# Kernel tuning notes

Hardware: AMD Instinct MI355X
Metric: run time of the kernel (lower is better)

The kernel has to match this reference:

```python
import jax, jax.numpy as jnp
import numpy as np

B, L = 1, 2048
D_MODEL, D_STATE, D_CONV, EXPAND = 512, 16, 4, 2
D_INNER = D_MODEL * EXPAND
EPS = 1e-10  # clamp used by the torch reference


def setup_inputs() -> dict:
    key = jax.random.key(0)
    ks = jax.random.split(key, 8)
    s = lambda fan: 1.0 / np.sqrt(fan)
    x = jax.random.normal(ks[0], (B, L, D_MODEL), jnp.float32)
    # Weights stored in (in, out) layout: y = x @ W  (equivalent to torch Linear with W.T)
    W_in = jax.random.normal(ks[1], (D_MODEL, 2 * D_INNER), jnp.float32) * s(D_MODEL)
    conv_w = jax.random.normal(ks[2], (D_INNER, 1, D_CONV), jnp.float32) * s(D_CONV)  # depthwise (O, I/groups, K)
    conv_b = jax.random.normal(ks[3], (D_INNER,), jnp.float32) * 0.01
    W_xproj = jax.random.normal(ks[4], (D_INNER, 2 * D_STATE + 1), jnp.float32) * s(D_INNER)
    dt_w = jax.random.normal(ks[5], (D_INNER,), jnp.float32) * 0.1  # Linear(1, d_inner) weight, squeezed
    dt_b = jax.random.normal(ks[6], (D_INNER,), jnp.float32) * 0.1 - 2.0  # keep delta smallish
    A_log = jnp.log(jnp.arange(1, D_STATE + 1, dtype=jnp.float32))
    D = jnp.ones((D_INNER,), jnp.float32)
    W_out = jax.random.normal(ks[7], (D_INNER, D_MODEL), jnp.float32) * s(D_INNER)
    return {"x": x, "W_in": W_in, "conv_w": conv_w, "conv_b": conv_b,
            "W_xproj": W_xproj, "dt_w": dt_w, "dt_b": dt_b,
            "A_log": A_log, "D": D, "W_out": W_out}


def reference(x, W_in, conv_w, conv_b, W_xproj, dt_w, dt_b, A_log, D, W_out):
    d_inner, _, d_conv = conv_w.shape
    d_state = A_log.shape[0]

    xz = x @ W_in                                    # (B, L, 2*d_inner)
    xs, z = jnp.split(xz, 2, axis=-1)

    # Depthwise causal conv1d: left-pad d_conv-1 == torch pad-both + truncate to L
    xc = jnp.transpose(xs, (0, 2, 1))                # (B, d_inner, L)
    xc = jax.lax.conv_general_dilated(
        xc, conv_w, window_strides=(1,), padding=[(d_conv - 1, 0)],
        feature_group_count=d_inner,
        dimension_numbers=("NCH", "OIH", "NCH")) + conv_b[None, :, None]
    xs = jax.nn.silu(jnp.transpose(xc, (0, 2, 1)))   # (B, L, d_inner)

    xp = xs @ W_xproj                                # (B, L, 2*d_state+1)
    delta = jax.nn.softplus(xp[..., 0:1] * dt_w + dt_b)  # (B, L, d_inner)
    Bp = xp[..., 1:1 + d_state]                      # (B, L, d_state)
    Cp = xp[..., 1 + d_state:]                       # (B, L, d_state)
    A = -jnp.exp(A_log)                              # (d_state,)

    # --- parallel selective scan via cumulative log-sum (faithful to source) ---
    A_bar = jnp.exp(delta[..., None] * A)                            # (B,L,Di,S)
    BX = delta[..., None] * Bp[:, :, None, :] * xs[..., None]        # (B,L,Di,S)
    log_A_bar = jnp.log(jnp.maximum(A_bar, EPS))
    A_cumsum = jnp.exp(jnp.cumsum(log_A_bar, axis=1))
    A_shift = jnp.concatenate([jnp.ones_like(A_cumsum[:, :1]), A_cumsum[:, :-1]], axis=1)
    weighted_BX = BX / jnp.maximum(A_shift, EPS)
    h = A_cumsum * jnp.cumsum(weighted_BX, axis=1) / jnp.maximum(A_bar, EPS)
    y = jnp.einsum("bls,blds->bld", Cp, h) + D * xs                  # (B,L,Di)

    y = y * jax.nn.silu(z)
    return y @ W_out                                                  # (B,L,D)
```

## Files before the change

kernel.cpp:

```cpp
#include <hip/hip_runtime.h>
#include <hip/hip_bf16.h>


#define L_SEQ 2048
#define DM 512
#define DI 1024
#define DS 16
#define NXP 33
#define EPS 1e-10f
#define RCPEPS 1e10f
#define LOG2E 1.44269504088896340736f
#define LN2 0.69314718055994530942f
#define LOG2EPS -33.219280948873623478f

typedef __hip_bfloat16 bf16;
typedef __attribute__((ext_vector_type(8))) short bf16x8v;
typedef __attribute__((ext_vector_type(4))) float f32x4v;
typedef __attribute__((ext_vector_type(4))) unsigned int u32x4v;

__device__ __forceinline__ void st1(float* p, float v) { *p = v; }
__device__ __forceinline__ void st1(bf16* p, float v) { *p = __float2bfloat16(v); }

__device__ __forceinline__ float fexp2(float x) { return __builtin_amdgcn_exp2f(x); }
__device__ __forceinline__ float frcp(float x) { return __builtin_amdgcn_rcpf(x); }

__device__ __forceinline__ void load8(const float* p, float* v) {
  float4 a = *(const float4*)p;
  float4 b = *(const float4*)(p + 4);
  v[0] = a.x; v[1] = a.y; v[2] = a.z; v[3] = a.w;
  v[4] = b.x; v[5] = b.y; v[6] = b.z; v[7] = b.w;
}

__global__ __launch_bounds__(256)
void prep_kernel(const float* __restrict__ W_in, bf16* __restrict__ WinT,
                 const float* __restrict__ x, bf16* __restrict__ xbf) {
  __shared__ float tile[32][33];
  int b = blockIdx.x;
  if (b < 1024) {
    int c0 = (b & 63) * 32, r0 = (b >> 6) * 32;
    int tx = threadIdx.x & 31, ty = threadIdx.x >> 5;
#pragma unroll
    for (int i = 0; i < 4; ++i) {
      int rr = ty + i * 8;
      tile[rr][tx] = W_in[(size_t)(r0 + rr) * (2 * DI) + c0 + tx];
    }
    __syncthreads();
#pragma unroll
    for (int i = 0; i < 4; ++i) {
      int cc = ty + i * 8;
      WinT[(size_t)(c0 + cc) * DM + r0 + tx] = __float2bfloat16(tile[tx][cc]);
    }
  } else {
    int i = (b - 1024) * 256 + threadIdx.x;
    float v[8];
    load8(x + (size_t)i * 8, v);
    bf16 o[8];
#pragma unroll
    for (int j = 0; j < 8; ++j) o[j] = __float2bfloat16(v[j]);
    *(uint4*)(xbf + (size_t)i * 8) = *(uint4*)o;
  }
}

template <int WM, int WN, typename TC>
__global__ __launch_bounds__(256)
void gemm_gl(const bf16* __restrict__ A, const bf16* __restrict__ BT,
             TC* __restrict__ C, int K, int lda, int ldc) {
  constexpr int BM = 2 * WM * 16, BN = 2 * WN * 16;
  __shared__ __align__(16) bf16 As[2][BM * 32];
  __shared__ __align__(16) bf16 Bs[2][BN * 32];
  const int tid = threadIdx.x;
  const int wave = tid >> 6, lane = tid & 63;
  const int q = lane >> 4, r = lane & 15;
  const int wr = wave >> 1, wc = wave & 1;
  const int row0 = blockIdx.y * BM, col0 = blockIdx.x * BN;
  f32x4v acc[WM][WN] = {};
  const int nt = K / 32;

  auto stage = [&](int buf, int t) {
    int k0 = t * 32;
#pragma unroll
    for (int i = 0; i < BM / 64; ++i) {
      int slot = tid + i * 256;
      int row = slot >> 2, seg = slot & 3;
      __builtin_amdgcn_global_load_lds(
          (const __attribute__((address_space(1))) void*)(
              A + (size_t)(row0 + row) * lda + k0 + seg * 8),
          (__attribute__((address_space(3))) void*)&As[buf][row * 32 + seg * 8],
          16, 0, 0);
    }
#pragma unroll
    for (int i = 0; i < BN / 64; ++i) {
      int slot = tid + i * 256;
      int row = slot >> 2, seg = slot & 3;
      __builtin_amdgcn_global_load_lds(
          (const __attribute__((address_space(1))) void*)(
              BT + (size_t)(col0 + row) * K + k0 + seg * 8),
          (__attribute__((address_space(3))) void*)&Bs[buf][row * 32 + seg * 8],
          16, 0, 0);
    }
  };

  stage(0, 0);
  __syncthreads();
  int cur = 0;
  for (int t = 0; t < nt; ++t) {
    if (t + 1 < nt) stage(cur ^ 1, t + 1);
    bf16x8v a[WM], b[WN];
#pragma unroll
    for (int m = 0; m < WM; ++m)
      a[m] = *(const bf16x8v*)&As[cur][(wr * WM * 16 + m * 16 + r) * 32 + q * 8];
#pragma unroll
    for (int n = 0; n < WN; ++n)
      b[n] = *(const bf16x8v*)&Bs[cur][(wc * WN * 16 + n * 16 + r) * 32 + q * 8];
#pragma unroll
    for (int m = 0; m < WM; ++m)
#pragma unroll
      for (int n = 0; n < WN; ++n)
        acc[m][n] = __builtin_amdgcn_mfma_f32_16x16x32_bf16(a[m], b[n],
                                                            acc[m][n], 0, 0, 0);
    __syncthreads();
    cur ^= 1;
  }
#pragma unroll
  for (int m = 0; m < WM; ++m)
#pragma unroll
    for (int n = 0; n < WN; ++n)
#pragma unroll
      for (int reg = 0; reg < 4; ++reg) {
        int mm = row0 + wr * WM * 16 + m * 16 + q * 4 + reg;
        int nn = col0 + wc * WN * 16 + n * 16 + r;
        st1(C + (size_t)mm * ldc + nn, acc[m][n][reg]);
      }
}

__global__ __launch_bounds__(256)
void gemm_xproj_sk(const bf16* __restrict__ A, const float* __restrict__ Wx,
                   float* __restrict__ xpcT) {
  __shared__ __align__(16) bf16 As[64 * 40];
  __shared__ __align__(16) bf16 Bs[64 * 40];
  const int tid = threadIdx.x;
  const int wave = tid >> 6, lane = tid & 63;
  const int q = lane >> 4, r = lane & 15;
  const int row0 = blockIdx.y * 64;
  const int kb = blockIdx.x * 128;
  const int srow = tid >> 2, sseg = tid & 3;
  f32x4v acc[4] = {};
  for (int k0 = kb; k0 < kb + 128; k0 += 32) {
    *(uint4*)&As[srow * 40 + sseg * 8] =
        *(const uint4*)(A + (size_t)(row0 + srow) * DI + k0 + sseg * 8);
    int k = tid >> 3, n0 = (tid & 7) * 8;
#pragma unroll
    for (int j = 0; j < 8; ++j) {
      int n = n0 + j;
      float v = (n < NXP) ? Wx[(size_t)(k0 + k) * NXP + n] : 0.f;
      Bs[n * 40 + k] = __float2bfloat16(v);
    }
    __syncthreads();
    bf16x8v a = *(const bf16x8v*)&As[(wave * 16 + r) * 40 + q * 8];
#pragma unroll
    for (int j = 0; j < 4; ++j) {
      bf16x8v b = *(const bf16x8v*)&Bs[(j * 16 + r) * 40 + q * 8];
      acc[j] = __builtin_amdgcn_mfma_f32_16x16x32_bf16(a, b, acc[j], 0, 0, 0);
    }
    __syncthreads();
  }
#pragma unroll
  for (int j = 0; j < 4; ++j)
#pragma unroll
    for (int reg = 0; reg < 4; ++reg) {
      int m = row0 + wave * 16 + q * 4 + reg;
      int n = j * 16 + r;
      if (n < NXP) atomicAdd(&xpcT[(size_t)n * L_SEQ + m], acc[j][reg]);
    }
}

__global__ __launch_bounds__(256)
void conv_silu_dual(const bf16* __restrict__ xz, const float* __restrict__ conv_w,
                    const float* __restrict__ conv_b, bf16* __restrict__ xs,
                    bf16* __restrict__ xsT, float* __restrict__ xpcT) {
  __shared__ bf16 tile[67][72];
  __shared__ bf16 sout[64][72];
  const int tid = threadIdx.x;
  const int d0 = blockIdx.x * 64, l0 = blockIdx.y * 64;
  {
    int zb = blockIdx.y * gridDim.x + blockIdx.x;
    if (tid < 132) xpcT[(size_t)zb * 132 + tid] = 0.f;
  }
  for (int slot = tid; slot < 67 * 8; slot += 256) {
    int rr = slot >> 3, seg = slot & 7;
    int l = l0 - 3 + rr;
    uint4 v = {0, 0, 0, 0};
    if (l >= 0) v = *(const uint4*)(xz + (size_t)l * (2 * DI) + d0 + seg * 8);
    *(uint4*)&tile[rr][seg * 8] = v;
  }
  __syncthreads();
  {
    int lr = tid >> 3, c0t = (tid & 7) * 8;
#pragma unroll
    for (int half = 0; half < 2; ++half) {
      int lrow = lr + half * 32;
      bf16 o[8];
#pragma unroll
      for (int j = 0; j < 8; ++j) {
        int c = c0t + j;
        float acc = conv_b[d0 + c];
#pragma unroll
        for (int k = 0; k < 4; ++k)
          acc = fmaf(__bfloat162float(tile[lrow + k][c]), conv_w[(d0 + c) * 4 + k], acc);
        float v = acc / (1.f + __expf(-acc));
        o[j] = __float2bfloat16(v);
        sout[c][lrow] = o[j];
      }
      *(uint4*)(xs + (size_t)(l0 + lrow) * DI + d0 + c0t) = *(uint4*)o;
    }
  }
  __syncthreads();
  for (int slot = tid; slot < 64 * 8; slot += 256) {
    int dd = slot >> 3, seg = slot & 7;
    *(uint4*)(xsT + (size_t)(d0 + dd) * L_SEQ + l0 + seg * 8) =
        *(uint4*)&sout[dd][seg * 8];
  }
}

__global__ __launch_bounds__(256)
void gate_wt_kernel(const bf16* __restrict__ yT, const bf16* __restrict__ zbuf,
                    int ldz, bf16* __restrict__ ys,
                    const float* __restrict__ W_out, bf16* __restrict__ WoutT) {
  __shared__ bf16 tile[64][72];
  __shared__ float ttile[32][33];
  if (blockIdx.y >= 16) {
    int tb = (blockIdx.y - 16) * 32 + blockIdx.x;
    int c0 = (tb & 15) * 32, r0 = (tb >> 4) * 32;
    int tx = threadIdx.x & 31, ty = threadIdx.x >> 5;
#pragma unroll
    for (int i = 0; i < 4; ++i) {
      int rr = ty + i * 8;
      ttile[rr][tx] = W_out[(size_t)(r0 + rr) * DM + c0 + tx];
    }
    __syncthreads();
#pragma unroll
    for (int i = 0; i < 4; ++i) {
      int cc = ty + i * 8;
      WoutT[(size_t)(c0 + cc) * DI + r0 + tx] = __float2bfloat16(ttile[tx][cc]);
    }
    return;
  }
  int d0 = blockIdx.y * 64, l0 = blockIdx.x * 64;
#pragma unroll
  for (int it = 0; it < 2; ++it) {
    int slot = threadIdx.x + it * 256;
    int dd = slot >> 3, seg = slot & 7;
    *(uint4*)&tile[dd][seg * 8] = *(const uint4*)(yT + (size_t)(d0 + dd) * L_SEQ + l0 + seg * 8);
  }
  __syncthreads();
#pragma unroll
  for (int it = 0; it < 2; ++it) {
    int slot = threadIdx.x + it * 256;
    int ll = slot >> 3, seg = slot & 7;
    bf16 zt[8];
    *(uint4*)zt = *(const uint4*)(zbuf + (size_t)(l0 + ll) * ldz + d0 + seg * 8);
    bf16 o[8];
#pragma unroll
    for (int j = 0; j < 8; ++j) {
      float yv = __bfloat162float(tile[seg * 8 + j][ll]);
      float zv = __bfloat162float(zt[j]);
      o[j] = __float2bfloat16(yv * zv * frcp(1.f + fexp2(-zv * LOG2E)));
    }
    *(uint4*)(ys + (size_t)(l0 + ll) * DI + d0 + seg * 8) = *(uint4*)o;
  }
}

#define LC 512
#define NW 16
#define SPW 32
#define PSX 513
#define LCP 516

__global__ __launch_bounds__(1024)
void scan_kernel(bf16* __restrict__ xsT, const float* __restrict__ xpcT,
                 const float* __restrict__ dt_w, const float* __restrict__ dt_b,
                 const float* __restrict__ A_log, const float* __restrict__ Dvec) {
  __shared__ float sxpT[NXP * PSX];
  __shared__ float sdt[4 * LCP], sg[4 * LCP], sxs[4 * LCP];
  __shared__ float sys[4 * LCP];
  __shared__ float Wtot[NW][64], Vtot[NW][64];
  const int tid = threadIdx.x;
  const int wave = tid >> 6, lane = tid & 63;
  const int s = lane & 15, dl = lane >> 4;
  const int d0 = blockIdx.x * 4;
  const int base = wave * SPW;
  const float As2 = -expf(A_log[s]) * LOG2E;
  const float Dd = Dvec[d0 + dl];
  float dtw[4], dtb[4];
#pragma unroll
  for (int c = 0; c < 4; ++c) {
    dtw[c] = dt_w[d0 + c];
    dtb[c] = dt_b[d0 + c];
  }
  float cs2_carry = 0.f, S_carry = 0.f;
  for (int l0 = 0; l0 < L_SEQ; l0 += LC) {
    for (int idx = tid; idx < NXP * LC; idx += 1024) {
      int u = __builtin_amdgcn_readfirstlane(idx & ~63);
      int j = u >> 9, lb = u & (LC - 1);
      const float* gp = xpcT + (size_t)j * L_SEQ + l0 + lb + lane;
      __builtin_amdgcn_global_load_lds(
          (const __attribute__((address_space(1))) void*)gp,
          (__attribute__((address_space(3))) void*)&sxpT[j * PSX + lb], 4, 0, 0);
    }
    for (int slot = tid; slot < 4 * (LC / 8); slot += 1024) {
      int c = slot >> 6, seg = slot & 63;
      bf16 tmp[8];
      *(uint4*)tmp = *(const uint4*)(xsT + (size_t)(d0 + c) * L_SEQ + l0 + seg * 8);
#pragma unroll
      for (int j = 0; j < 8; ++j) sxs[c * LCP + seg * 8 + j] = __bfloat162float(tmp[j]);
    }
    __syncthreads();
    for (int idx = tid; idx < 4 * LC; idx += 1024) {
      int c = idx >> 9, i = idx & (LC - 1);
      float x0 = sxpT[i];
      float a = fmaf(x0, dtw[c], dtb[c]);
      float dt = __log2f(1.f + fexp2(a * LOG2E)) * LN2;
      sdt[c * LCP + i] = dt;
      sg[c * LCP + i] = dt * sxs[c * LCP + i];
    }
    __syncthreads();
    float P[SPW];
    float Wl = 0.f;
#pragma unroll
    for (int k = 0; k < SPW; ++k) {
      float u = sdt[dl * LCP + base + k] * As2;
      P[k] = Wl;
      Wl += fmaxf(u, LOG2EPS);
    }
    Wtot[wave][lane] = Wl;
    __syncthreads();
    float O = cs2_carry, Wall = 0.f;
    for (int w = 0; w < NW; ++w) {
      float t = Wtot[w][lane];
      if (w < wave) O += t;
      Wall += t;
    }
    float Vl = 0.f;
#pragma unroll
    for (int k = 0; k < SPW; ++k) {
      float rcpA = fminf(fexp2(-(O + P[k])), RCPEPS);
      float gb = sg[dl * LCP + base + k] * sxpT[(1 + s) * PSX + base + k];
      Vl = fmaf(gb, rcpA, Vl);
    }
    Vtot[wave][lane] = Vl;
    __syncthreads();
    float SO = S_carry, Vall = 0.f;
    for (int w = 0; w < NW; ++w) {
      float tv = Vtot[w][lane];
      if (w < wave) SO += tv;
      Vall += tv;
    }
    float S = SO;
#pragma unroll
    for (int k = 0; k < SPW; ++k) {
      float xk = O + P[k];
      float rcpA = fminf(fexp2(-xk), RCPEPS);
      float aprev = fexp2(xk);
      float gb = sg[dl * LCP + base + k] * sxpT[(1 + s) * PSX + base + k];
      S = fmaf(gb, rcpA, S);
      float h = aprev * S;
      float contrib = sxpT[(17 + s) * PSX + base + k] * h;
      contrib += __shfl_xor(contrib, 8);
      contrib += __shfl_xor(contrib, 4);
      contrib += __shfl_xor(contrib, 2);
      contrib += __shfl_xor(contrib, 1);
      if (s == 0)
        sys[dl * LCP + base + k] = contrib + Dd * sxs[dl * LCP + base + k];
    }
    cs2_carry += Wall;
    S_carry += Vall;
    __syncthreads();
    for (int slot = tid; slot < 4 * (LC / 8); slot += 1024) {
      int c = slot >> 6, seg = slot & 63;
      bf16 tmp[8];
#pragma unroll
      for (int j = 0; j < 8; ++j) tmp[j] = __float2bfloat16(sys[c * LCP + seg * 8 + j]);
      u32x4v vv;
      vv.x = ((unsigned int*)tmp)[0]; vv.y = ((unsigned int*)tmp)[1];
      vv.z = ((unsigned int*)tmp)[2]; vv.w = ((unsigned int*)tmp)[3];
      __builtin_nontemporal_store(vv,
          (u32x4v*)(xsT + (size_t)(d0 + c) * L_SEQ + l0 + seg * 8));
    }
  }
}

extern "C" void kernel_launch(void* const* d_in, const int* in_sizes, int n_in,
                              void* d_out, int out_size, void* d_ws, size_t ws_size,
                              hipStream_t stream) {
  const float* x       = (const float*)d_in[0];
  const float* W_in    = (const float*)d_in[1];
  const float* conv_w  = (const float*)d_in[2];
  const float* conv_b  = (const float*)d_in[3];
  const float* W_xproj = (const float*)d_in[4];
  const float* dt_w    = (const float*)d_in[5];
  const float* dt_b    = (const float*)d_in[6];
  const float* A_log   = (const float*)d_in[7];
  const float* Dvec    = (const float*)d_in[8];
  const float* W_out   = (const float*)d_in[9];
  float* out = (float*)d_out;

  char* ws = (char*)d_ws;
  const size_t MB = 1024 * 1024;
  bf16* xz    = (bf16*)(ws);
  bf16* buf1  = (bf16*)(ws + 8 * MB);
  bf16* WinT  = (bf16*)(ws + 12 * MB);
  bf16* xbf   = (bf16*)(ws + 14 * MB);
  bf16* xsT   = (bf16*)(ws + 12 * MB);
  float* xpcT = (float*)(ws + 16 * MB);
  bf16* WoutT = (bf16*)(ws + 16 * MB);

  prep_kernel<<<dim3(1536), 256, 0, stream>>>(W_in, WinT, x, xbf);
  gemm_gl<4, 4, bf16><<<dim3(2 * DI / 128, L_SEQ / 128), 256, 0, stream>>>(
      xbf, WinT, xz, DM, DM, 2 * DI);
  conv_silu_dual<<<dim3(DI / 64, L_SEQ / 64), 256, 0, stream>>>(
      xz, conv_w, conv_b, buf1, xsT, xpcT);
  gemm_xproj_sk<<<dim3(8, L_SEQ / 64), 256, 0, stream>>>(buf1, W_xproj, xpcT);
  scan_kernel<<<DI / 4, 1024, 0, stream>>>(xsT, xpcT, dt_w, dt_b, A_log, Dvec);
  gate_wt_kernel<<<dim3(L_SEQ / 64, 2 * DI / 64), 256, 0, stream>>>(
      xsT, xz + DI, 2 * DI, buf1, W_out, WoutT);
  gemm_gl<2, 2, float><<<dim3(DM / 64, L_SEQ / 64), 256, 0, stream>>>(
      buf1, WoutT, out, DI, DI, DM);
}
```

Before: 191.5 us.

## Fuse x_proj GEMV into conv+SiLU kernel and move xpcT zeroing to prep

The x_proj projection is now computed inside the conv/SiLU kernel from the transposed SiLU output already in shared memory. Each block does a 64-channel partial dot product in FP32 with W_xproj staged in LDS, and adds it atomically into xpcT. This removes the separate split-K MFMA kernel launch and the row-major xs write and read-back. Zeroing of xpcT moves into extra blocks of the prep kernel. In exchange there are more atomic adds per output (16 channel blocks instead of 8 k-splits), scalar FMA replaces MFMA, and LDS use per block rises.

```diff
diff --git a/kernel.cpp b/kernel.cpp
--- a/kernel.cpp
+++ b/kernel.cpp
@@ -33,7 +33,8 @@
 
 __global__ __launch_bounds__(256)
 void prep_kernel(const float* __restrict__ W_in, bf16* __restrict__ WinT,
-                 const float* __restrict__ x, bf16* __restrict__ xbf) {
+                 const float* __restrict__ x, bf16* __restrict__ xbf,
+                 float* __restrict__ xpcT) {
   __shared__ float tile[32][33];
   int b = blockIdx.x;
   if (b < 1024) {
@@ -50,7 +51,7 @@
       int cc = ty + i * 8;
       WinT[(size_t)(c0 + cc) * DM + r0 + tx] = __float2bfloat16(tile[tx][cc]);
     }
-  } else {
+  } else if (b < 1536) {
     int i = (b - 1024) * 256 + threadIdx.x;
     float v[8];
     load8(x + (size_t)i * 8, v);
@@ -58,6 +59,9 @@
 #pragma unroll
     for (int j = 0; j < 8; ++j) o[j] = __float2bfloat16(v[j]);
     *(uint4*)(xbf + (size_t)i * 8) = *(uint4*)o;
+  } else {
+    int i = (b - 1536) * 256 + threadIdx.x;
+    xpcT[i] = 0.f;
   }
 }
 
@@ -134,58 +138,16 @@
 }
 
 __global__ __launch_bounds__(256)
-void gemm_xproj_sk(const bf16* __restrict__ A, const float* __restrict__ Wx,
-                   float* __restrict__ xpcT) {
-  __shared__ __align__(16) bf16 As[64 * 40];
-  __shared__ __align__(16) bf16 Bs[64 * 40];
-  const int tid = threadIdx.x;
-  const int wave = tid >> 6, lane = tid & 63;
-  const int q = lane >> 4, r = lane & 15;
-  const int row0 = blockIdx.y * 64;
-  const int kb = blockIdx.x * 128;
-  const int srow = tid >> 2, sseg = tid & 3;
-  f32x4v acc[4] = {};
-  for (int k0 = kb; k0 < kb + 128; k0 += 32) {
-    *(uint4*)&As[srow * 40 + sseg * 8] =
-        *(const uint4*)(A + (size_t)(row0 + srow) * DI + k0 + sseg * 8);
-    int k = tid >> 3, n0 = (tid & 7) * 8;
-#pragma unroll
-    for (int j = 0; j < 8; ++j) {
-      int n = n0 + j;
-      float v = (n < NXP) ? Wx[(size_t)(k0 + k) * NXP + n] : 0.f;
-      Bs[n * 40 + k] = __float2bfloat16(v);
-    }
-    __syncthreads();
-    bf16x8v a = *(const bf16x8v*)&As[(wave * 16 + r) * 40 + q * 8];
-#pragma unroll
-    for (int j = 0; j < 4; ++j) {
-      bf16x8v b = *(const bf16x8v*)&Bs[(j * 16 + r) * 40 + q * 8];
-      acc[j] = __builtin_amdgcn_mfma_f32_16x16x32_bf16(a, b, acc[j], 0, 0, 0);
-    }
-    __syncthreads();
-  }
-#pragma unroll
-  for (int j = 0; j < 4; ++j)
-#pragma unroll
-    for (int reg = 0; reg < 4; ++reg) {
-      int m = row0 + wave * 16 + q * 4 + reg;
-      int n = j * 16 + r;
-      if (n < NXP) atomicAdd(&xpcT[(size_t)n * L_SEQ + m], acc[j][reg]);
-    }
-}
-
-__global__ __launch_bounds__(256)
-void conv_silu_dual(const bf16* __restrict__ xz, const float* __restrict__ conv_w,
-                    const float* __restrict__ conv_b, bf16* __restrict__ xs,
-                    bf16* __restrict__ xsT, float* __restrict__ xpcT) {
+void conv_silu_xproj(const bf16* __restrict__ xz, const float* __restrict__ conv_w,
+                     const float* __restrict__ conv_b, bf16* __restrict__ xsT,
+                     const float* __restrict__ Wx, float* __restrict__ xpcT) {
   __shared__ bf16 tile[67][72];
   __shared__ bf16 sout[64][72];
+  __shared__ float sWx[64 * NXP];
   const int tid = threadIdx.x;
   const int d0 = blockIdx.x * 64, l0 = blockIdx.y * 64;
-  {
-    int zb = blockIdx.y * gridDim.x + blockIdx.x;
-    if (tid < 132) xpcT[(size_t)zb * 132 + tid] = 0.f;
-  }
+  for (int idx = tid; idx < 64 * NXP; idx += 256)
+    sWx[idx] = Wx[(size_t)d0 * NXP + idx];
   for (int slot = tid; slot < 67 * 8; slot += 256) {
     int rr = slot >> 3, seg = slot & 7;
     int l = l0 - 3 + rr;
@@ -199,7 +161,6 @@
 #pragma unroll
     for (int half = 0; half < 2; ++half) {
       int lrow = lr + half * 32;
-      bf16 o[8];
 #pragma unroll
       for (int j = 0; j < 8; ++j) {
         int c = c0t + j;
@@ -208,10 +169,8 @@
         for (int k = 0; k < 4; ++k)
           acc = fmaf(__bfloat162float(tile[lrow + k][c]), conv_w[(d0 + c) * 4 + k], acc);
         float v = acc / (1.f + __expf(-acc));
-        o[j] = __float2bfloat16(v);
-        sout[c][lrow] = o[j];
+        sout[c][lrow] = __float2bfloat16(v);
       }
-      *(uint4*)(xs + (size_t)(l0 + lrow) * DI + d0 + c0t) = *(uint4*)o;
     }
   }
   __syncthreads();
@@ -219,6 +178,23 @@
     int dd = slot >> 3, seg = slot & 7;
     *(uint4*)(xsT + (size_t)(d0 + dd) * L_SEQ + l0 + seg * 8) =
         *(uint4*)&sout[dd][seg * 8];
+  }
+  {
+    const int jg = tid >> 6, l = tid & 63;
+    float acc[9] = {};
+    for (int d = 0; d < 64; ++d) {
+      float xl = __bfloat162float(sout[d][l]);
+#pragma unroll
+      for (int m = 0; m < 9; ++m) {
+        int j = jg + 4 * m;
+        if (j < NXP) acc[m] = fmaf(xl, sWx[d * NXP + j], acc[m]);
+      }
+    }
+#pragma unroll
+    for (int m = 0; m < 9; ++m) {
+      int j = jg + 4 * m;
+      if (j < NXP) atomicAdd(&xpcT[(size_t)j * L_SEQ + l0 + l], acc[m]);
+    }
   }
 }
 
@@ -414,12 +390,11 @@
   float* xpcT = (float*)(ws + 16 * MB);
   bf16* WoutT = (bf16*)(ws + 16 * MB);
 
-  prep_kernel<<<dim3(1536), 256, 0, stream>>>(W_in, WinT, x, xbf);
+  prep_kernel<<<dim3(1800), 256, 0, stream>>>(W_in, WinT, x, xbf, xpcT);
   gemm_gl<4, 4, bf16><<<dim3(2 * DI / 128, L_SEQ / 128), 256, 0, stream>>>(
       xbf, WinT, xz, DM, DM, 2 * DI);
-  conv_silu_dual<<<dim3(DI / 64, L_SEQ / 64), 256, 0, stream>>>(
-      xz, conv_w, conv_b, buf1, xsT, xpcT);
-  gemm_xproj_sk<<<dim3(8, L_SEQ / 64), 256, 0, stream>>>(buf1, W_xproj, xpcT);
+  conv_silu_xproj<<<dim3(DI / 64, L_SEQ / 64), 256, 0, stream>>>(
+      xz, conv_w, conv_b, xsT, W_xproj, xpcT);
   scan_kernel<<<DI / 4, 1024, 0, stream>>>(xsT, xpcT, dt_w, dt_b, A_log, Dvec);
   gate_wt_kernel<<<dim3(L_SEQ / 64, 2 * DI / 64), 256, 0, stream>>>(
       xsT, xz + DI, 2 * DI, buf1, W_out, WoutT);
```

Measured after the change: 196.9 us. 2.8% more time.

## Fuse SiLU gate into scan epilogue and drop gate/transpose kernel

Applied to the files above, without the earlier changes.

The first GEMM now writes the x half row-major and the z half transposed (zT). The scan epilogue applies y*silu(z) directly, so the separate gate_wt kernel goes away. The output GEMM reads the transposed ys and converts W_out from fp32 on the fly inside a new simpler GEMM. This saves one launch and a full round trip of y and z through memory. In exchange, the output GEMM uses scalar transposing LDS stores and no double buffering, and it reconverts W_out in every block.

```diff
diff --git a/kernel.cpp b/kernel.cpp
--- a/kernel.cpp
+++ b/kernel.cpp
@@ -18,9 +18,6 @@
 typedef __attribute__((ext_vector_type(4))) float f32x4v;
 typedef __attribute__((ext_vector_type(4))) unsigned int u32x4v;
 
-__device__ __forceinline__ void st1(float* p, float v) { *p = v; }
-__device__ __forceinline__ void st1(bf16* p, float v) { *p = __float2bfloat16(v); }
-
 __device__ __forceinline__ float fexp2(float x) { return __builtin_amdgcn_exp2f(x); }
 __device__ __forceinline__ float frcp(float x) { return __builtin_amdgcn_rcpf(x); }
 
@@ -61,11 +58,10 @@
   }
 }
 
-template <int WM, int WN, typename TC>
 __global__ __launch_bounds__(256)
-void gemm_gl(const bf16* __restrict__ A, const bf16* __restrict__ BT,
-             TC* __restrict__ C, int K, int lda, int ldc) {
-  constexpr int BM = 2 * WM * 16, BN = 2 * WN * 16;
+void gemm1_kernel(const bf16* __restrict__ A, const bf16* __restrict__ BT,
+                  bf16* __restrict__ xc, bf16* __restrict__ zT) {
+  constexpr int WM = 4, WN = 4, BM = 128, BN = 128, K = DM;
   __shared__ __align__(16) bf16 As[2][BM * 32];
   __shared__ __align__(16) bf16 Bs[2][BN * 32];
   const int tid = threadIdx.x;
@@ -84,7 +80,7 @@
       int row = slot >> 2, seg = slot & 3;
       __builtin_amdgcn_global_load_lds(
           (const __attribute__((address_space(1))) void*)(
-              A + (size_t)(row0 + row) * lda + k0 + seg * 8),
+              A + (size_t)(row0 + row) * DM + k0 + seg * 8),
           (__attribute__((address_space(3))) void*)&As[buf][row * 32 + seg * 8],
           16, 0, 0);
     }
@@ -121,16 +117,30 @@
     __syncthreads();
     cur ^= 1;
   }
-#pragma unroll
-  for (int m = 0; m < WM; ++m)
-#pragma unroll
-    for (int n = 0; n < WN; ++n)
-#pragma unroll
-      for (int reg = 0; reg < 4; ++reg) {
-        int mm = row0 + wr * WM * 16 + m * 16 + q * 4 + reg;
-        int nn = col0 + wc * WN * 16 + n * 16 + r;
-        st1(C + (size_t)mm * ldc + nn, acc[m][n][reg]);
+  if (col0 < DI) {
+#pragma unroll
+    for (int m = 0; m < WM; ++m)
+#pragma unroll
+      for (int n = 0; n < WN; ++n)
+#pragma unroll
+        for (int reg = 0; reg < 4; ++reg) {
+          int mm = row0 + wr * WM * 16 + m * 16 + q * 4 + reg;
+          int nn = col0 + wc * WN * 16 + n * 16 + r;
+          xc[(size_t)mm * DI + nn] = __float2bfloat16(acc[m][n][reg]);
+        }
+  } else {
+#pragma unroll
+    for (int m = 0; m < WM; ++m)
+#pragma unroll
+      for (int n = 0; n < WN; ++n) {
+        int mm = row0 + wr * WM * 16 + m * 16 + q * 4;
+        int nn = col0 - DI + wc * WN * 16 + n * 16 + r;
+        bf16 o[4];
+#pragma unroll
+        for (int reg = 0; reg < 4; ++reg) o[reg] = __float2bfloat16(acc[m][n][reg]);
+        *(uint2*)(zT + (size_t)nn * L_SEQ + mm) = *(uint2*)o;
       }
+  }
 }
 
 __global__ __launch_bounds__(256)
@@ -175,7 +185,7 @@
 }
 
 __global__ __launch_bounds__(256)
-void conv_silu_dual(const bf16* __restrict__ xz, const float* __restrict__ conv_w,
+void conv_silu_dual(const bf16* __restrict__ xc, const float* __restrict__ conv_w,
                     const float* __restrict__ conv_b, bf16* __restrict__ xs,
                     bf16* __restrict__ xsT, float* __restrict__ xpcT) {
   __shared__ bf16 tile[67][72];
@@ -190,7 +200,7 @@
     int rr = slot >> 3, seg = slot & 7;
     int l = l0 - 3 + rr;
     uint4 v = {0, 0, 0, 0};
-    if (l >= 0) v = *(const uint4*)(xz + (size_t)l * (2 * DI) + d0 + seg * 8);
+    if (l >= 0) v = *(const uint4*)(xc + (size_t)l * DI + d0 + seg * 8);
     *(uint4*)&tile[rr][seg * 8] = v;
   }
   __syncthreads();
@@ -222,54 +232,6 @@
   }
 }
 
-__global__ __launch_bounds__(256)
-void gate_wt_kernel(const bf16* __restrict__ yT, const bf16* __restrict__ zbuf,
-                    int ldz, bf16* __restrict__ ys,
-                    const float* __restrict__ W_out, bf16* __restrict__ WoutT) {
-  __shared__ bf16 tile[64][72];
-  __shared__ float ttile[32][33];
-  if (blockIdx.y >= 16) {
-    int tb = (blockIdx.y - 16) * 32 + blockIdx.x;
-    int c0 = (tb & 15) * 32, r0 = (tb >> 4) * 32;
-    int tx = threadIdx.x & 31, ty = threadIdx.x >> 5;
-#pragma unroll
-    for (int i = 0; i < 4; ++i) {
-      int rr = ty + i * 8;
-      ttile[rr][tx] = W_out[(size_t)(r0 + rr) * DM + c0 + tx];
-    }
-    __syncthreads();
-#pragma unroll
-    for (int i = 0; i < 4; ++i) {
-      int cc = ty + i * 8;
-      WoutT[(size_t)(c0 + cc) * DI + r0 + tx] = __float2bfloat16(ttile[tx][cc]);
-    }
-    return;
-  }
-  int d0 = blockIdx.y * 64, l0 = blockIdx.x * 64;
-#pragma unroll
-  for (int it = 0; it < 2; ++it) {
-    int slot = threadIdx.x + it * 256;
-    int dd = slot >> 3, seg = slot & 7;
-    *(uint4*)&tile[dd][seg * 8] = *(const uint4*)(yT + (size_t)(d0 + dd) * L_SEQ + l0 + seg * 8);
-  }
-  __syncthreads();
-#pragma unroll
-  for (int it = 0; it < 2; ++it) {
-    int slot = threadIdx.x + it * 256;
-    int ll = slot >> 3, seg = slot & 7;
-    bf16 zt[8];
-    *(uint4*)zt = *(const uint4*)(zbuf + (size_t)(l0 + ll) * ldz + d0 + seg * 8);
-    bf16 o[8];
-#pragma unroll
-    for (int j = 0; j < 8; ++j) {
-      float yv = __bfloat162float(tile[seg * 8 + j][ll]);
-      float zv = __bfloat162float(zt[j]);
-      o[j] = __float2bfloat16(yv * zv * frcp(1.f + fexp2(-zv * LOG2E)));
-    }
-    *(uint4*)(ys + (size_t)(l0 + ll) * DI + d0 + seg * 8) = *(uint4*)o;
-  }
-}
-
 #define LC 512
 #define NW 16
 #define SPW 32
@@ -278,6 +240,7 @@
 
 __global__ __launch_bounds__(1024)
 void scan_kernel(bf16* __restrict__ xsT, const float* __restrict__ xpcT,
+                 const bf16* __restrict__ zT,
                  const float* __restrict__ dt_w, const float* __restrict__ dt_b,
                  const float* __restrict__ A_log, const float* __restrict__ Dvec) {
   __shared__ float sxpT[NXP * PSX];
@@ -377,9 +340,15 @@
     __syncthreads();
     for (int slot = tid; slot < 4 * (LC / 8); slot += 1024) {
       int c = slot >> 6, seg = slot & 63;
+      bf16 zt[8];
+      *(uint4*)zt = *(const uint4*)(zT + (size_t)(d0 + c) * L_SEQ + l0 + seg * 8);
       bf16 tmp[8];
 #pragma unroll
-      for (int j = 0; j < 8; ++j) tmp[j] = __float2bfloat16(sys[c * LCP + seg * 8 + j]);
+      for (int j = 0; j < 8; ++j) {
+        float yv = sys[c * LCP + seg * 8 + j];
+        float zv = __bfloat162float(zt[j]);
+        tmp[j] = __float2bfloat16(yv * zv * frcp(1.f + fexp2(-zv * LOG2E)));
+      }
       u32x4v vv;
       vv.x = ((unsigned int*)tmp)[0]; vv.y = ((unsigned int*)tmp)[1];
       vv.z = ((unsigned int*)tmp)[2]; vv.w = ((unsigned int*)tmp)[3];
@@ -387,6 +356,59 @@
           (u32x4v*)(xsT + (size_t)(d0 + c) * L_SEQ + l0 + seg * 8));
     }
   }
+}
+
+__global__ __launch_bounds__(256)
+void gemm2_kernel(const bf16* __restrict__ ysT, const float* __restrict__ W_out,
+                  float* __restrict__ out) {
+  __shared__ __align__(16) bf16 As[64 * 34];
+  __shared__ __align__(16) bf16 Bs[64 * 34];
+  const int tid = threadIdx.x;
+  const int wave = tid >> 6, lane = tid & 63;
+  const int q = lane >> 4, r = lane & 15;
+  const int wr = wave >> 1, wc = wave & 1;
+  const int row0 = blockIdx.y * 64, col0 = blockIdx.x * 64;
+  const int dr = tid >> 3, sg = tid & 7;
+  f32x4v acc[2][2] = {};
+  for (int k0 = 0; k0 < DI; k0 += 32) {
+    {
+      bf16 t[8];
+      *(uint4*)t = *(const uint4*)(ysT + (size_t)(k0 + dr) * L_SEQ + row0 + sg * 8);
+#pragma unroll
+      for (int i = 0; i < 8; ++i) As[(sg * 8 + i) * 34 + dr] = t[i];
+    }
+    {
+      float v[8];
+      load8(W_out + (size_t)(k0 + dr) * DM + col0 + sg * 8, v);
+#pragma unroll
+      for (int i = 0; i < 8; ++i) Bs[(sg * 8 + i) * 34 + dr] = __float2bfloat16(v[i]);
+    }
+    __syncthreads();
+    bf16x8v a[2], b[2];
+#pragma unroll
+    for (int m = 0; m < 2; ++m)
+      a[m] = *(const bf16x8v*)&As[(wr * 32 + m * 16 + r) * 34 + q * 8];
+#pragma unroll
+    for (int n = 0; n < 2; ++n)
+      b[n] = *(const bf16x8v*)&Bs[(wc * 32 + n * 16 + r) * 34 + q * 8];
+#pragma unroll
+    for (int m = 0; m < 2; ++m)
+#pragma unroll
+      for (int n = 0; n < 2; ++n)
+        acc[m][n] = __builtin_amdgcn_mfma_f32_16x16x32_bf16(a[m], b[n],
+                                                            acc[m][n], 0, 0, 0);
+    __syncthreads();
+  }
+#pragma unroll
+  for (int m = 0; m < 2; ++m)
+#pragma unroll
+    for (int n = 0; n < 2; ++n)
+#pragma unroll
+      for (int reg = 0; reg < 4; ++reg) {
+        int mm = row0 + wr * 32 + m * 16 + q * 4 + reg;
+        int nn = col0 + wc * 32 + n * 16 + r;
+        out[(size_t)mm * DM + nn] = acc[m][n][reg];
+      }
 }
 
 extern "C" void kernel_launch(void* const* d_in, const int* in_sizes, int n_in,
@@ -406,23 +428,20 @@
 
   char* ws = (char*)d_ws;
   const size_t MB = 1024 * 1024;
-  bf16* xz    = (bf16*)(ws);
+  bf16* xc    = (bf16*)(ws);
+  bf16* zT    = (bf16*)(ws + 4 * MB);
   bf16* buf1  = (bf16*)(ws + 8 * MB);
   bf16* WinT  = (bf16*)(ws + 12 * MB);
   bf16* xbf   = (bf16*)(ws + 14 * MB);
   bf16* xsT   = (bf16*)(ws + 12 * MB);
   float* xpcT = (float*)(ws + 16 * MB);
-  bf16* WoutT = (bf16*)(ws + 16 * MB);
 
   prep_kernel<<<dim3(1536), 256, 0, stream>>>(W_in, WinT, x, xbf);
-  gemm_gl<4, 4, bf16><<<dim3(2 * DI / 128, L_SEQ / 128), 256, 0, stream>>>(
-      xbf, WinT, xz, DM, DM, 2 * DI);
+  gemm1_kernel<<<dim3(2 * DI / 128, L_SEQ / 128), 256, 0, stream>>>(
+      xbf, WinT, xc, zT);
   conv_silu_dual<<<dim3(DI / 64, L_SEQ / 64), 256, 0, stream>>>(
-      xz, conv_w, conv_b, buf1, xsT, xpcT);
+      xc, conv_w, conv_b, buf1, xsT, xpcT);
   gemm_xproj_sk<<<dim3(8, L_SEQ / 64), 256, 0, stream>>>(buf1, W_xproj, xpcT);
-  scan_kernel<<<DI / 4, 1024, 0, stream>>>(xsT, xpcT, dt_w, dt_b, A_log, Dvec);
-  gate_wt_kernel<<<dim3(L_SEQ / 64, 2 * DI / 64), 256, 0, stream>>>(
-      xsT, xz + DI, 2 * DI, buf1, W_out, WoutT);
-  gemm_gl<2, 2, float><<<dim3(DM / 64, L_SEQ / 64), 256, 0, stream>>>(
-      buf1, WoutT, out, DI, DI, DM);
-}
+  scan_kernel<<<DI / 4, 1024, 0, stream>>>(xsT, xpcT, zT, dt_w, dt_b, A_log, Dvec);
+  gemm2_kernel<<<dim3(DM / 64, L_SEQ / 64), 256, 0, stream>>>(xsT, W_out, out);
+}
```

Measured after the change: 198.5 us. 1.04x slower.

## Fuse conv, xproj, scan and gate into one cooperative persistent kernel

Applied to the files above, without the earlier changes.

Merges the conv+SiLU, x-projection GEMM, selective scan and gating/W_out transpose kernels into a single cooperative launch of 256 blocks of 1024 threads, with grid syncs between phases. Each block runs four 256-thread sub-tiles for the elementwise phases and reuses one shared-memory buffer across phases. The goal is to remove three kernel launch boundaries and their tail idle time. The trade-off is poorer per-phase occupancy: only one quarter of the threads work during the xproj phase, the block size is large, and grid syncs add cost.

```diff
diff --git a/kernel.cpp b/kernel.cpp
--- a/kernel.cpp
+++ b/kernel.cpp
@@ -1,5 +1,8 @@
 #include <hip/hip_runtime.h>
 #include <hip/hip_bf16.h>
+#include <hip/hip_cooperative_groups.h>
+
+namespace cg = cooperative_groups;
 
 
 #define L_SEQ 2048
@@ -133,258 +136,282 @@
       }
 }
 
-__global__ __launch_bounds__(256)
-void gemm_xproj_sk(const bf16* __restrict__ A, const float* __restrict__ Wx,
-                   float* __restrict__ xpcT) {
-  __shared__ __align__(16) bf16 As[64 * 40];
-  __shared__ __align__(16) bf16 Bs[64 * 40];
-  const int tid = threadIdx.x;
-  const int wave = tid >> 6, lane = tid & 63;
-  const int q = lane >> 4, r = lane & 15;
-  const int row0 = blockIdx.y * 64;
-  const int kb = blockIdx.x * 128;
-  const int srow = tid >> 2, sseg = tid & 3;
-  f32x4v acc[4] = {};
-  for (int k0 = kb; k0 < kb + 128; k0 += 32) {
-    *(uint4*)&As[srow * 40 + sseg * 8] =
-        *(const uint4*)(A + (size_t)(row0 + srow) * DI + k0 + sseg * 8);
-    int k = tid >> 3, n0 = (tid & 7) * 8;
-#pragma unroll
-    for (int j = 0; j < 8; ++j) {
-      int n = n0 + j;
-      float v = (n < NXP) ? Wx[(size_t)(k0 + k) * NXP + n] : 0.f;
-      Bs[n * 40 + k] = __float2bfloat16(v);
-    }
-    __syncthreads();
-    bf16x8v a = *(const bf16x8v*)&As[(wave * 16 + r) * 40 + q * 8];
-#pragma unroll
-    for (int j = 0; j < 4; ++j) {
-      bf16x8v b = *(const bf16x8v*)&Bs[(j * 16 + r) * 40 + q * 8];
-      acc[j] = __builtin_amdgcn_mfma_f32_16x16x32_bf16(a, b, acc[j], 0, 0, 0);
-    }
-    __syncthreads();
-  }
-#pragma unroll
-  for (int j = 0; j < 4; ++j)
-#pragma unroll
-    for (int reg = 0; reg < 4; ++reg) {
-      int m = row0 + wave * 16 + q * 4 + reg;
-      int n = j * 16 + r;
-      if (n < NXP) atomicAdd(&xpcT[(size_t)n * L_SEQ + m], acc[j][reg]);
-    }
-}
-
-__global__ __launch_bounds__(256)
-void conv_silu_dual(const bf16* __restrict__ xz, const float* __restrict__ conv_w,
-                    const float* __restrict__ conv_b, bf16* __restrict__ xs,
-                    bf16* __restrict__ xsT, float* __restrict__ xpcT) {
-  __shared__ bf16 tile[67][72];
-  __shared__ bf16 sout[64][72];
-  const int tid = threadIdx.x;
-  const int d0 = blockIdx.x * 64, l0 = blockIdx.y * 64;
-  {
-    int zb = blockIdx.y * gridDim.x + blockIdx.x;
-    if (tid < 132) xpcT[(size_t)zb * 132 + tid] = 0.f;
-  }
-  for (int slot = tid; slot < 67 * 8; slot += 256) {
-    int rr = slot >> 3, seg = slot & 7;
-    int l = l0 - 3 + rr;
-    uint4 v = {0, 0, 0, 0};
-    if (l >= 0) v = *(const uint4*)(xz + (size_t)l * (2 * DI) + d0 + seg * 8);
-    *(uint4*)&tile[rr][seg * 8] = v;
-  }
-  __syncthreads();
-  {
-    int lr = tid >> 3, c0t = (tid & 7) * 8;
-#pragma unroll
-    for (int half = 0; half < 2; ++half) {
-      int lrow = lr + half * 32;
-      bf16 o[8];
-#pragma unroll
-      for (int j = 0; j < 8; ++j) {
-        int c = c0t + j;
-        float acc = conv_b[d0 + c];
-#pragma unroll
-        for (int k = 0; k < 4; ++k)
-          acc = fmaf(__bfloat162float(tile[lrow + k][c]), conv_w[(d0 + c) * 4 + k], acc);
-        float v = acc / (1.f + __expf(-acc));
-        o[j] = __float2bfloat16(v);
-        sout[c][lrow] = o[j];
-      }
-      *(uint4*)(xs + (size_t)(l0 + lrow) * DI + d0 + c0t) = *(uint4*)o;
-    }
-  }
-  __syncthreads();
-  for (int slot = tid; slot < 64 * 8; slot += 256) {
-    int dd = slot >> 3, seg = slot & 7;
-    *(uint4*)(xsT + (size_t)(d0 + dd) * L_SEQ + l0 + seg * 8) =
-        *(uint4*)&sout[dd][seg * 8];
-  }
-}
-
-__global__ __launch_bounds__(256)
-void gate_wt_kernel(const bf16* __restrict__ yT, const bf16* __restrict__ zbuf,
-                    int ldz, bf16* __restrict__ ys,
-                    const float* __restrict__ W_out, bf16* __restrict__ WoutT) {
-  __shared__ bf16 tile[64][72];
-  __shared__ float ttile[32][33];
-  if (blockIdx.y >= 16) {
-    int tb = (blockIdx.y - 16) * 32 + blockIdx.x;
-    int c0 = (tb & 15) * 32, r0 = (tb >> 4) * 32;
-    int tx = threadIdx.x & 31, ty = threadIdx.x >> 5;
-#pragma unroll
-    for (int i = 0; i < 4; ++i) {
-      int rr = ty + i * 8;
-      ttile[rr][tx] = W_out[(size_t)(r0 + rr) * DM + c0 + tx];
-    }
-    __syncthreads();
-#pragma unroll
-    for (int i = 0; i < 4; ++i) {
-      int cc = ty + i * 8;
-      WoutT[(size_t)(c0 + cc) * DI + r0 + tx] = __float2bfloat16(ttile[tx][cc]);
-    }
-    return;
-  }
-  int d0 = blockIdx.y * 64, l0 = blockIdx.x * 64;
-#pragma unroll
-  for (int it = 0; it < 2; ++it) {
-    int slot = threadIdx.x + it * 256;
-    int dd = slot >> 3, seg = slot & 7;
-    *(uint4*)&tile[dd][seg * 8] = *(const uint4*)(yT + (size_t)(d0 + dd) * L_SEQ + l0 + seg * 8);
-  }
-  __syncthreads();
-#pragma unroll
-  for (int it = 0; it < 2; ++it) {
-    int slot = threadIdx.x + it * 256;
-    int ll = slot >> 3, seg = slot & 7;
-    bf16 zt[8];
-    *(uint4*)zt = *(const uint4*)(zbuf + (size_t)(l0 + ll) * ldz + d0 + seg * 8);
-    bf16 o[8];
-#pragma unroll
-    for (int j = 0; j < 8; ++j) {
-      float yv = __bfloat162float(tile[seg * 8 + j][ll]);
-      float zv = __bfloat162float(zt[j]);
-      o[j] = __float2bfloat16(yv * zv * frcp(1.f + fexp2(-zv * LOG2E)));
-    }
-    *(uint4*)(ys + (size_t)(l0 + ll) * DI + d0 + seg * 8) = *(uint4*)o;
-  }
-}
-
 #define LC 512
 #define NW 16
 #define SPW 32
 #define PSX 513
 #define LCP 516
 
+struct ConvSh { bf16 tile[67][72]; bf16 sout[64][72]; };
+struct XpSh   { bf16 As[64 * 40]; bf16 Bs[64 * 40]; };
+struct GateSh { bf16 tile[64][72]; float ttile[32][33]; };
+struct ScanSh {
+  float sxpT[NXP * PSX];
+  float sdt[4 * LCP]; float sg[4 * LCP]; float sxs[4 * LCP]; float sys[4 * LCP];
+  float Wtot[NW][64]; float Vtot[NW][64];
+};
+
 __global__ __launch_bounds__(1024)
-void scan_kernel(bf16* __restrict__ xsT, const float* __restrict__ xpcT,
-                 const float* __restrict__ dt_w, const float* __restrict__ dt_b,
-                 const float* __restrict__ A_log, const float* __restrict__ Dvec) {
-  __shared__ float sxpT[NXP * PSX];
-  __shared__ float sdt[4 * LCP], sg[4 * LCP], sxs[4 * LCP];
-  __shared__ float sys[4 * LCP];
-  __shared__ float Wtot[NW][64], Vtot[NW][64];
+void fused_mid(const bf16* __restrict__ xz, const float* __restrict__ conv_w,
+               const float* __restrict__ conv_b, bf16* __restrict__ xsbuf,
+               bf16* __restrict__ xsT, float* __restrict__ xpcT,
+               const float* __restrict__ Wx,
+               const float* __restrict__ dt_w, const float* __restrict__ dt_b,
+               const float* __restrict__ A_log, const float* __restrict__ Dvec,
+               const float* __restrict__ W_out, bf16* __restrict__ WoutT) {
+  __shared__ __align__(16) char shraw[sizeof(ScanSh)];
   const int tid = threadIdx.x;
-  const int wave = tid >> 6, lane = tid & 63;
-  const int s = lane & 15, dl = lane >> 4;
-  const int d0 = blockIdx.x * 4;
-  const int base = wave * SPW;
-  const float As2 = -expf(A_log[s]) * LOG2E;
-  const float Dd = Dvec[d0 + dl];
-  float dtw[4], dtb[4];
-#pragma unroll
-  for (int c = 0; c < 4; ++c) {
-    dtw[c] = dt_w[d0 + c];
-    dtb[c] = dt_b[d0 + c];
-  }
-  float cs2_carry = 0.f, S_carry = 0.f;
-  for (int l0 = 0; l0 < L_SEQ; l0 += LC) {
-    for (int idx = tid; idx < NXP * LC; idx += 1024) {
-      int u = __builtin_amdgcn_readfirstlane(idx & ~63);
-      int j = u >> 9, lb = u & (LC - 1);
-      const float* gp = xpcT + (size_t)j * L_SEQ + l0 + lb + lane;
-      __builtin_amdgcn_global_load_lds(
-          (const __attribute__((address_space(1))) void*)gp,
-          (__attribute__((address_space(3))) void*)&sxpT[j * PSX + lb], 4, 0, 0);
-    }
-    for (int slot = tid; slot < 4 * (LC / 8); slot += 1024) {
-      int c = slot >> 6, seg = slot & 63;
-      bf16 tmp[8];
-      *(uint4*)tmp = *(const uint4*)(xsT + (size_t)(d0 + c) * L_SEQ + l0 + seg * 8);
-#pragma unroll
-      for (int j = 0; j < 8; ++j) sxs[c * LCP + seg * 8 + j] = __bfloat162float(tmp[j]);
+  const int tid_l = tid & 255, g = tid >> 8;
+  const int bid = blockIdx.x;
+  cg::grid_group gridg = cg::this_grid();
+
+  {
+    ConvSh& cs = reinterpret_cast<ConvSh*>(shraw)[g];
+    int u = g * 256 + bid;
+    bool act = u < 512;
+    int d0 = (u & 15) * 64, l0 = (u >> 4) * 64;
+    if (act && tid_l < 132) xpcT[(size_t)u * 132 + tid_l] = 0.f;
+    if (act) {
+      for (int slot = tid_l; slot < 67 * 8; slot += 256) {
+        int rr = slot >> 3, seg = slot & 7;
+        int l = l0 - 3 + rr;
+        uint4 v = {0, 0, 0, 0};
+        if (l >= 0) v = *(const uint4*)(xz + (size_t)l * (2 * DI) + d0 + seg * 8);
+        *(uint4*)&cs.tile[rr][seg * 8] = v;
+      }
     }
     __syncthreads();
-    for (int idx = tid; idx < 4 * LC; idx += 1024) {
-      int c = idx >> 9, i = idx & (LC - 1);
-      float x0 = sxpT[i];
-      float a = fmaf(x0, dtw[c], dtb[c]);
-      float dt = __log2f(1.f + fexp2(a * LOG2E)) * LN2;
-      sdt[c * LCP + i] = dt;
-      sg[c * LCP + i] = dt * sxs[c * LCP + i];
+    if (act) {
+      int lr = tid_l >> 3, c0t = (tid_l & 7) * 8;
+#pragma unroll
+      for (int half = 0; half < 2; ++half) {
+        int lrow = lr + half * 32;
+        bf16 o[8];
+#pragma unroll
+        for (int j = 0; j < 8; ++j) {
+          int c = c0t + j;
+          float acc = conv_b[d0 + c];
+#pragma unroll
+          for (int k = 0; k < 4; ++k)
+            acc = fmaf(__bfloat162float(cs.tile[lrow + k][c]),
+                       conv_w[(d0 + c) * 4 + k], acc);
+          float v = acc / (1.f + __expf(-acc));
+          o[j] = __float2bfloat16(v);
+          cs.sout[c][lrow] = o[j];
+        }
+        *(uint4*)(xsbuf + (size_t)(l0 + lrow) * DI + d0 + c0t) = *(uint4*)o;
+      }
     }
     __syncthreads();
-    float P[SPW];
-    float Wl = 0.f;
-#pragma unroll
-    for (int k = 0; k < SPW; ++k) {
-      float u = sdt[dl * LCP + base + k] * As2;
-      P[k] = Wl;
-      Wl += fmaxf(u, LOG2EPS);
-    }
-    Wtot[wave][lane] = Wl;
+    if (act) {
+      for (int slot = tid_l; slot < 64 * 8; slot += 256) {
+        int dd = slot >> 3, seg = slot & 7;
+        *(uint4*)(xsT + (size_t)(d0 + dd) * L_SEQ + l0 + seg * 8) =
+            *(uint4*)&cs.sout[dd][seg * 8];
+      }
+    }
+  }
+  gridg.sync();
+  {
+    XpSh& xp = reinterpret_cast<XpSh*>(shraw)[0];
+    bool act = (g == 0);
+    int row0 = (bid >> 3) * 64, kb = (bid & 7) * 128;
+    const int wv = tid_l >> 6, lane = tid_l & 63;
+    const int q = lane >> 4, r = lane & 15;
+    const int srow = tid_l >> 2, sseg = tid_l & 3;
+    f32x4v acc[4] = {};
+    for (int step = 0; step < 4; ++step) {
+      int k0 = kb + step * 32;
+      if (act) {
+        *(uint4*)&xp.As[srow * 40 + sseg * 8] =
+            *(const uint4*)(xsbuf + (size_t)(row0 + srow) * DI + k0 + sseg * 8);
+        int k = tid_l >> 3, n0 = (tid_l & 7) * 8;
+#pragma unroll
+        for (int j = 0; j < 8; ++j) {
+          int n = n0 + j;
+          float v = (n < NXP) ? Wx[(size_t)(k0 + k) * NXP + n] : 0.f;
+          xp.Bs[n * 40 + k] = __float2bfloat16(v);
+        }
+      }
+      __syncthreads();
+      if (act) {
+        bf16x8v a = *(const bf16x8v*)&xp.As[(wv * 16 + r) * 40 + q * 8];
+#pragma unroll
+        for (int j = 0; j < 4; ++j) {
+          bf16x8v b = *(const bf16x8v*)&xp.Bs[(j * 16 + r) * 40 + q * 8];
+          acc[j] = __builtin_amdgcn_mfma_f32_16x16x32_bf16(a, b, acc[j], 0, 0, 0);
+        }
+      }
+      __syncthreads();
+    }
+    if (act) {
+#pragma unroll
+      for (int j = 0; j < 4; ++j)
+#pragma unroll
+        for (int reg = 0; reg < 4; ++reg) {
+          int m = row0 + wv * 16 + q * 4 + reg;
+          int n = j * 16 + r;
+          if (n < NXP) atomicAdd(&xpcT[(size_t)n * L_SEQ + m], acc[j][reg]);
+        }
+    }
+  }
+  gridg.sync();
+  {
+    ScanSh& ss = *reinterpret_cast<ScanSh*>(shraw);
+    const int wave = tid >> 6, lane = tid & 63;
+    const int s = lane & 15, dl = lane >> 4;
+    const int d0 = bid * 4;
+    const int base = wave * SPW;
+    const float As2 = -expf(A_log[s]) * LOG2E;
+    const float Dd = Dvec[d0 + dl];
+    float dtw[4], dtb[4];
+#pragma unroll
+    for (int c = 0; c < 4; ++c) {
+      dtw[c] = dt_w[d0 + c];
+      dtb[c] = dt_b[d0 + c];
+    }
+    float cs2_carry = 0.f, S_carry = 0.f;
+    for (int l0 = 0; l0 < L_SEQ; l0 += LC) {
+      for (int idx = tid; idx < NXP * LC; idx += 1024) {
+        int u = __builtin_amdgcn_readfirstlane(idx & ~63);
+        int j = u >> 9, lb = u & (LC - 1);
+        const float* gp = xpcT + (size_t)j * L_SEQ + l0 + lb + lane;
+        __builtin_amdgcn_global_load_lds(
+            (const __attribute__((address_space(1))) void*)gp,
+            (__attribute__((address_space(3))) void*)&ss.sxpT[j * PSX + lb], 4, 0, 0);
+      }
+      for (int slot = tid; slot < 4 * (LC / 8); slot += 1024) {
+        int c = slot >> 6, seg = slot & 63;
+        bf16 tmp[8];
+        *(uint4*)tmp = *(const uint4*)(xsT + (size_t)(d0 + c) * L_SEQ + l0 + seg * 8);
+#pragma unroll
+        for (int j = 0; j < 8; ++j) ss.sxs[c * LCP + seg * 8 + j] = __bfloat162float(tmp[j]);
+      }
+      __syncthreads();
+      for (int idx = tid; idx < 4 * LC; idx += 1024) {
+        int c = idx >> 9, i = idx & (LC - 1);
+        float x0 = ss.sxpT[i];
+        float a = fmaf(x0, dtw[c], dtb[c]);
+        float dt = __log2f(1.f + fexp2(a * LOG2E)) * LN2;
+        ss.sdt[c * LCP + i] = dt;
+        ss.sg[c * LCP + i] = dt * ss.sxs[c * LCP + i];
+      }
+      __syncthreads();
+      float P[SPW];
+      float Wl = 0.f;
+#pragma unroll
+      for (int k = 0; k < SPW; ++k) {
+        float u = ss.sdt[dl * LCP + base + k] * As2;
+        P[k] = Wl;
+        Wl += fmaxf(u, LOG2EPS);
+      }
+      ss.Wtot[wave][lane] = Wl;
+      __syncthreads();
+      float O = cs2_carry, Wall = 0.f;
+      for (int w = 0; w < NW; ++w) {
+        float t = ss.Wtot[w][lane];
+        if (w < wave) O += t;
+        Wall += t;
+      }
+      float Vl = 0.f;
+#pragma unroll
+      for (int k = 0; k < SPW; ++k) {
+        float rcpA = fminf(fexp2(-(O + P[k])), RCPEPS);
+        float gb = ss.sg[dl * LCP + base + k] * ss.sxpT[(1 + s) * PSX + base + k];
+        Vl = fmaf(gb, rcpA, Vl);
+      }
+      ss.Vtot[wave][lane] = Vl;
+      __syncthreads();
+      float SO = S_carry, Vall = 0.f;
+      for (int w = 0; w < NW; ++w) {
+        float tv = ss.Vtot[w][lane];
+        if (w < wave) SO += tv;
+        Vall += tv;
+      }
+      float S = SO;
+#pragma unroll
+      for (int k = 0; k < SPW; ++k) {
+        float xk = O + P[k];
+        float rcpA = fminf(fexp2(-xk), RCPEPS);
+        float aprev = fexp2(xk);
+        float gb = ss.sg[dl * LCP + base + k] * ss.sxpT[(1 + s) * PSX + base + k];
+        S = fmaf(gb, rcpA, S);
+        float h = aprev * S;
+        float contrib = ss.sxpT[(17 + s) * PSX + base + k] * h;
+        contrib += __shfl_xor(contrib, 8);
+        contrib += __shfl_xor(contrib, 4);
+        contrib += __shfl_xor(contrib, 2);
+        contrib += __shfl_xor(contrib, 1);
+        if (s == 0)
+          ss.sys[dl * LCP + base + k] = contrib + Dd * ss.sxs[dl * LCP + base + k];
+      }
+      cs2_carry += Wall;
+      S_carry += Vall;
+      __syncthreads();
+      for (int slot = tid; slot < 4 * (LC / 8); slot += 1024) {
+        int c = slot >> 6, seg = slot & 63;
+        bf16 tmp[8];
+#pragma unroll
+        for (int j = 0; j < 8; ++j) tmp[j] = __float2bfloat16(ss.sys[c * LCP + seg * 8 + j]);
+        u32x4v vv;
+        vv.x = ((unsigned int*)tmp)[0]; vv.y = ((unsigned int*)tmp)[1];
+        vv.z = ((unsigned int*)tmp)[2]; vv.w = ((unsigned int*)tmp)[3];
+        __builtin_nontemporal_store(vv,
+            (u32x4v*)(xsT + (size_t)(d0 + c) * L_SEQ + l0 + seg * 8));
+      }
+    }
+  }
+  gridg.sync();
+  {
+    GateSh& gs = reinterpret_cast<GateSh*>(shraw)[g];
+    int u = g * 256 + bid;
+    int lx = u & 31, y = u >> 5;
+    if (y >= 16) {
+      int tb = (y - 16) * 32 + lx;
+      int c0 = (tb & 15) * 32, r0 = (tb >> 4) * 32;
+      int tx = tid_l & 31, ty = tid_l >> 5;
+#pragma unroll
+      for (int i = 0; i < 4; ++i) {
+        int rr = ty + i * 8;
+        gs.ttile[rr][tx] = W_out[(size_t)(r0 + rr) * DM + c0 + tx];
+      }
+    } else {
+      int d0 = y * 64, l0 = lx * 64;
+#pragma unroll
+      for (int it = 0; it < 2; ++it) {
+        int slot = tid_l + it * 256;
+        int dd = slot >> 3, seg = slot & 7;
+        *(uint4*)&gs.tile[dd][seg * 8] =
+            *(const uint4*)(xsT + (size_t)(d0 + dd) * L_SEQ + l0 + seg * 8);
+      }
+    }
     __syncthreads();
-    float O = cs2_carry, Wall = 0.f;
-    for (int w = 0; w < NW; ++w) {
-      float t = Wtot[w][lane];
-      if (w < wave) O += t;
-      Wall += t;
-    }
-    float Vl = 0.f;
-#pragma unroll
-    for (int k = 0; k < SPW; ++k) {
-      float rcpA = fminf(fexp2(-(O + P[k])), RCPEPS);
-      float gb = sg[dl * LCP + base + k] * sxpT[(1 + s) * PSX + base + k];
-      Vl = fmaf(gb, rcpA, Vl);
-    }
-    Vtot[wave][lane] = Vl;
-    __syncthreads();
-    float SO = S_carry, Vall = 0.f;
-    for (int w = 0; w < NW; ++w) {
-      float tv = Vtot[w][lane];
-      if (w < wave) SO += tv;
-      Vall += tv;
-    }
-    float S = SO;
-#pragma unroll
-    for (int k = 0; k < SPW; ++k) {
-      float xk = O + P[k];
-      float rcpA = fminf(fexp2(-xk), RCPEPS);
-      float aprev = fexp2(xk);
-      float gb = sg[dl * LCP + base + k] * sxpT[(1 + s) * PSX + base + k];
-      S = fmaf(gb, rcpA, S);
-      float h = aprev * S;
-      float contrib = sxpT[(17 + s) * PSX + base + k] * h;
-      contrib += __shfl_xor(contrib, 8);
-      contrib += __shfl_xor(contrib, 4);
-      contrib += __shfl_xor(contrib, 2);
-      contrib += __shfl_xor(contrib, 1);
-      if (s == 0)
-        sys[dl * LCP + base + k] = contrib + Dd * sxs[dl * LCP + base + k];
-    }
-    cs2_carry += Wall;
-    S_carry += Vall;
-    __syncthreads();
-    for (int slot = tid; slot < 4 * (LC / 8); slot += 1024) {
-      int c = slot >> 6, seg = slot & 63;
-      bf16 tmp[8];
-#pragma unroll
-      for (int j = 0; j < 8; ++j) tmp[j] = __float2bfloat16(sys[c * LCP + seg * 8 + j]);
-      u32x4v vv;
-      vv.x = ((unsigned int*)tmp)[0]; vv.y = ((unsigned int*)tmp)[1];
-      vv.z = ((unsigned int*)tmp)[2]; vv.w = ((unsigned int*)tmp)[3];
-      __builtin_nontemporal_store(vv,
-          (u32x4v*)(xsT + (size_t)(d0 + c) * L_SEQ + l0 + seg * 8));
+    if (y >= 16) {
+      int tb = (y - 16) * 32 + lx;
+      int c0 = (tb & 15) * 32, r0 = (tb >> 4) * 32;
+      int tx = tid_l & 31, ty = tid_l >> 5;
+#pragma unroll
+      for (int i = 0; i < 4; ++i) {
+        int cc = ty + i * 8;
+        WoutT[(size_t)(c0 + cc) * DI + r0 + tx] = __float2bfloat16(gs.ttile[tx][cc]);
+      }
+    } else {
+      int d0 = y * 64, l0 = lx * 64;
+#pragma unroll
+      for (int it = 0; it < 2; ++it) {
+        int slot = tid_l + it * 256;
+        int ll = slot >> 3, seg = slot & 7;
+        bf16 zt[8];
+        *(uint4*)zt = *(const uint4*)(xz + DI + (size_t)(l0 + ll) * (2 * DI) + d0 + seg * 8);
+        bf16 o[8];
+#pragma unroll
+        for (int j = 0; j < 8; ++j) {
+          float yv = __bfloat162float(gs.tile[seg * 8 + j][ll]);
+          float zv = __bfloat162float(zt[j]);
+          o[j] = __float2bfloat16(yv * zv * frcp(1.f + fexp2(-zv * LOG2E)));
+        }
+        *(uint4*)(xsbuf + (size_t)(l0 + ll) * DI + d0 + seg * 8) = *(uint4*)o;
+      }
     }
   }
 }
@@ -417,12 +444,15 @@
   prep_kernel<<<dim3(1536), 256, 0, stream>>>(W_in, WinT, x, xbf);
   gemm_gl<4, 4, bf16><<<dim3(2 * DI / 128, L_SEQ / 128), 256, 0, stream>>>(
       xbf, WinT, xz, DM, DM, 2 * DI);
-  conv_silu_dual<<<dim3(DI / 64, L_SEQ / 64), 256, 0, stream>>>(
-      xz, conv_w, conv_b, buf1, xsT, xpcT);
-  gemm_xproj_sk<<<dim3(8, L_SEQ / 64), 256, 0, stream>>>(buf1, W_xproj, xpcT);
-  scan_kernel<<<DI / 4, 1024, 0, stream>>>(xsT, xpcT, dt_w, dt_b, A_log, Dvec);
-  gate_wt_kernel<<<dim3(L_SEQ / 64, 2 * DI / 64), 256, 0, stream>>>(
-      xsT, xz + DI, 2 * DI, buf1, W_out, WoutT);
+  {
+    void* kargs[] = {(void*)&xz,     (void*)&conv_w, (void*)&conv_b,
+                     (void*)&buf1,   (void*)&xsT,    (void*)&xpcT,
+                     (void*)&W_xproj,(void*)&dt_w,   (void*)&dt_b,
+                     (void*)&A_log,  (void*)&Dvec,   (void*)&W_out,
+                     (void*)&WoutT};
+    hipLaunchCooperativeKernel(fused_mid, dim3(256), dim3(1024), kargs, 0,
+                               stream);
+  }
   gemm_gl<2, 2, float><<<dim3(DM / 64, L_SEQ / 64), 256, 0, stream>>>(
       buf1, WoutT, out, DI, DI, DM);
 }
```

Result: slower. 401.0 us (+109.4%).
